# Optimization experiments

Hardware: AMD Instinct MI355X
Metric: run time of the kernel (lower is better)

Reference implementation:

```python
import jax, jax.numpy as jnp
import numpy as np

B, HW, C, D = 8, 65536, 64, 64  # batch, seq (H*W), channels, d_model
H = W = 256


def setup_inputs() -> dict:
    key = jax.random.key(0)
    ks = jax.random.split(key, 16)
    s = lambda k, shape, scale=0.05: jax.random.normal(k, shape, dtype=jnp.float32) * scale
    return {
        "x": jax.random.normal(ks[0], (B, HW, C), dtype=jnp.float32),
        "freq_map": jax.random.uniform(ks[1], (B, 1, H, W), dtype=jnp.float32),
        # proj_in: Linear(C, D)
        "W_in": s(ks[2], (C, D)), "b_in": s(ks[3], (D,)),
        # SimplifiedMambaKernel: in_proj Linear(D, 2D)
        "W_ip": s(ks[4], (D, 2 * D)), "b_ip": s(ks[5], (2 * D,)),
        # depthwise Conv1d(D, D, k=3, padding=1, groups=D): weight [D,1,3]
        "conv_w": s(ks[6], (D, 1, 3)), "conv_b": s(ks[7], (D,)),
        # mamba out_proj Linear(D, D)
        "W_op": s(ks[8], (D, D)), "b_op": s(ks[9], (D,)),
        # gate_net: Linear(1,16) -> ReLU -> Linear(16,C) -> Sigmoid
        "W_g1": s(ks[10], (1, 16)), "b_g1": s(ks[11], (16,)),
        "W_g2": s(ks[12], (16, C)), "b_g2": s(ks[13], (C,)),
        # proj_out: Linear(D, C)
        "W_out": s(ks[14], (D, C)), "b_out": s(ks[15], (C,)),
    }


def _mamba_kernel(feat, W_ip, b_ip, conv_w, conv_b, W_op, b_op):
    # feat: [B, L, D]
    x_and_res = feat @ W_ip + b_ip                      # [B, L, 2D]
    x_branch, res_branch = jnp.split(x_and_res, 2, axis=-1)
    xb = jnp.transpose(x_branch, (0, 2, 1))             # [B, D, L]
    xb = jax.lax.conv_general_dilated(
        xb, conv_w, window_strides=(1,), padding=[(1, 1)],
        feature_group_count=conv_w.shape[0],
        dimension_numbers=("NCH", "OIH", "NCH"))
    xb = xb + conv_b[None, :, None]
    x_branch = jnp.transpose(xb, (0, 2, 1))             # [B, L, D]
    out = jax.nn.silu(x_branch) * jax.nn.silu(res_branch)
    return out @ W_op + b_op


def reference(x, freq_map, W_in, b_in, W_ip, b_ip, conv_w, conv_b,
              W_op, b_op, W_g1, b_g1, W_g2, b_g2, W_out, b_out):
    feat = x @ W_in + b_in                              # [B, L, D]
    feat = _mamba_kernel(feat, W_ip, b_ip, conv_w, conv_b, W_op, b_op)
    feat_out = feat @ W_out + b_out                     # [B, L, C]
    # freq_map [B,1,H,W] -> flatten(2).permute(0,2,1) -> [B, L, 1]
    freq_flat = freq_map.reshape(freq_map.shape[0], 1, -1).transpose(0, 2, 1)
    gate = jax.nn.sigmoid(jax.nn.relu(freq_flat @ W_g1 + b_g1) @ W_g2 + b_g2)
    return feat_out * gate
```

## Files before the change

### kernel.cpp

```cpp
#include <hip/hip_runtime.h>
#include <hip/hip_bf16.h>

#define L_SEQ 65536
#define GROUPS_PER_B 256

typedef __attribute__((ext_vector_type(8))) short bf16x8;
typedef __attribute__((ext_vector_type(4))) short s16x4;
typedef __attribute__((ext_vector_type(4))) float f32x4;

#define WS_WFX   0
#define WS_W1R   24576
#define WS_W2T   32768
#define WS_WG2T  40960
#define WS_BX    43008
#define WS_BR    43264
#define WS_BC0   43520
#define WS_BC2   43776
#define WS_B2    44032

__device__ __forceinline__ short f2bf(float f) {
    __bf16 h = (__bf16)f;
    return __builtin_bit_cast(short, h);
}
__device__ __forceinline__ float fsigmoid(float x) {
    return __builtin_amdgcn_rcpf(1.0f + __builtin_amdgcn_exp2f(-1.44269504089f * x));
}

__global__ void prep_kernel(const float* __restrict__ W_in, const float* __restrict__ b_in,
                            const float* __restrict__ W_ip, const float* __restrict__ b_ip,
                            const float* __restrict__ conv_w, const float* __restrict__ conv_b,
                            const float* __restrict__ W_op, const float* __restrict__ b_op,
                            const float* __restrict__ W_g2,
                            const float* __restrict__ W_out, const float* __restrict__ b_out,
                            void* __restrict__ ws)
{
    short* wfx  = (short*)((char*)ws + WS_WFX);
    short* w1r  = (short*)((char*)ws + WS_W1R);
    short* w2t  = (short*)((char*)ws + WS_W2T);
    short* wg2t = (short*)((char*)ws + WS_WG2T);
    float* bx   = (float*)((char*)ws + WS_BX);
    float* br   = (float*)((char*)ws + WS_BR);
    float* bc0  = (float*)((char*)ws + WS_BC0);
    float* bc2  = (float*)((char*)ws + WS_BC2);
    float* b2   = (float*)((char*)ws + WS_B2);

    int tid = blockIdx.x * blockDim.x + threadIdx.x;
    if (tid < 12288) {
        int s = tid >> 12, rem = tid & 4095;
        int d = rem >> 6, c = rem & 63;
        float acc = 0.f;
        for (int e = 0; e < 64; ++e) acc += W_in[c*64 + e] * W_ip[e*128 + d];
        wfx[(s*64 + d)*64 + c] = f2bf(acc * conv_w[3*d + s]);
    } else if (tid < 16384) {
        int rem = tid - 12288; int d = rem >> 6, c = rem & 63;
        float acc = 0.f;
        for (int e = 0; e < 64; ++e) acc += W_in[c*64 + e] * W_ip[e*128 + 64 + d];
        w1r[d*64 + c] = f2bf(acc);
    } else if (tid < 20480) {
        int rem = tid - 16384; int cp = rem >> 6, d = rem & 63;
        float acc = 0.f;
        for (int e = 0; e < 64; ++e) acc += W_op[d*64 + e] * W_out[e*64 + cp];
        w2t[cp*64 + d] = f2bf(acc);
    } else if (tid < 21504) {
        int rem = tid - 20480; int c = rem >> 4, j = rem & 15;
        wg2t[c*16 + j] = f2bf(W_g2[j*64 + c]);
    } else if (tid < 21568) {
        int d = tid - 21504;
        float b1x = b_ip[d];
        for (int e = 0; e < 64; ++e) b1x += b_in[e] * W_ip[e*128 + d];
        bx[d] = b1x * (conv_w[3*d] + conv_w[3*d+1] + conv_w[3*d+2]) + conv_b[d];
    } else if (tid < 21632) {
        int d = tid - 21568;
        float s = b_ip[64 + d];
        for (int e = 0; e < 64; ++e) s += b_in[e] * W_ip[e*128 + 64 + d];
        br[d] = s;
    } else if (tid < 21696) {
        int d = tid - 21632;
        float b1x = b_ip[d];
        for (int e = 0; e < 64; ++e) b1x += b_in[e] * W_ip[e*128 + d];
        bc0[d] = b1x * conv_w[3*d];
    } else if (tid < 21760) {
        int d = tid - 21696;
        float b1x = b_ip[d];
        for (int e = 0; e < 64; ++e) b1x += b_in[e] * W_ip[e*128 + d];
        bc2[d] = b1x * conv_w[3*d + 2];
    } else if (tid < 21824) {
        int cp = tid - 21760;
        float s = b_out[cp];
        for (int e = 0; e < 64; ++e) s += b_op[e] * W_out[e*64 + cp];
        b2[cp] = s;
    }
}

__global__ __launch_bounds__(256, 4) void fgs_main(
    const float* __restrict__ x, const float* __restrict__ freq,
    const float* __restrict__ wg1, const float* __restrict__ bg1,
    const float* __restrict__ bg2,
    const void* __restrict__ ws, float* __restrict__ out)
{
    const short* wfx  = (const short*)((const char*)ws + WS_WFX);
    const short* w1r  = (const short*)((const char*)ws + WS_W1R);
    const short* w2t  = (const short*)((const char*)ws + WS_W2T);
    const short* wg2t = (const short*)((const char*)ws + WS_WG2T);
    const float* bxv  = (const float*)((const char*)ws + WS_BX);
    const float* brv  = (const float*)((const char*)ws + WS_BR);
    const float* bc0  = (const float*)((const char*)ws + WS_BC0);
    const float* bc2  = (const float*)((const char*)ws + WS_BC2);
    const float* b2   = (const float*)((const char*)ws + WS_B2);

    __shared__ short xs[2][66 * 64];
    __shared__ short ot[64][72];
    __shared__ short hl[2][64 * 16];

    const int bid   = blockIdx.x;
    const int batch = bid >> 8;
    const int tg    = bid & 255;
    const int base0 = tg << 8;

    const int lane = threadIdx.x & 63;
    const int w    = threadIdx.x >> 6;
    const int lr   = lane & 15;
    const int g    = lane >> 4;
    const int r    = 16*w + lr;
    const int c0   = 16*w + 4*g;

    const size_t brow0 = (size_t)batch * L_SEQ;

    bf16x8 awf[2][3], awr[2];
    #pragma unroll
    for (int kk = 0; kk < 2; ++kk) {
        #pragma unroll
        for (int s = 0; s < 3; ++s)
            awf[kk][s] = *(const bf16x8*)(wfx + (s*64 + 16*w + lr)*64 + 32*kk + 8*g);
        awr[kk] = *(const bf16x8*)(w1r + (16*w + lr)*64 + 32*kk + 8*g);
    }
    const float4 bbx = *(const float4*)(bxv + c0);
    const float4 bbr = *(const float4*)(brv + c0);
    const float4 wgv = *(const float4*)(wg1 + 4*g);
    const float4 bgv = *(const float4*)(bg1 + 4*g);

    float4 sa, sb, sc, sd; float sf;
    const int sro = threadIdx.x >> 2;
    const int sq  = (threadIdx.x & 3) * 16;

    auto stage_issue = [&](int tb) {
        int grow = tb + 1 + sro;
        bool v = ((unsigned)grow < (unsigned)L_SEQ);
        const float* p = x + (brow0 + (size_t)(v ? grow : 0)) * 64 + sq;
        sa = *(const float4*)(p);
        sb = *(const float4*)(p + 4);
        sc = *(const float4*)(p + 8);
        sd = *(const float4*)(p + 12);
        sf = freq[brow0 + tb + r];
    };
    auto stage_write = [&](short* xb, int tb) {
        int i = 2 + sro;
        int grow = tb + 1 + sro;
        bool v = ((unsigned)grow < (unsigned)L_SEQ);
        bf16x8 lo, hi;
        lo[0]=f2bf(sa.x); lo[1]=f2bf(sa.y); lo[2]=f2bf(sa.z); lo[3]=f2bf(sa.w);
        lo[4]=f2bf(sb.x); lo[5]=f2bf(sb.y); lo[6]=f2bf(sb.z); lo[7]=f2bf(sb.w);
        hi[0]=f2bf(sc.x); hi[1]=f2bf(sc.y); hi[2]=f2bf(sc.z); hi[3]=f2bf(sc.w);
        hi[4]=f2bf(sd.x); hi[5]=f2bf(sd.y); hi[6]=f2bf(sd.z); hi[7]=f2bf(sd.w);
        if (!v) { bf16x8 z = {}; lo = z; hi = z; }
        int cb = sq >> 3;
        int sw = i & 7;
        *(bf16x8*)&xb[i*64 + ((cb    ) ^ sw) * 8] = lo;
        *(bf16x8*)&xb[i*64 + ((cb + 1) ^ sw) * 8] = hi;
    };
    auto halo_copy = [&](short* xb, const short* xprev) {
        if (threadIdx.x < 16) {
            int ii = threadIdx.x >> 3;
            int cc = threadIdx.x & 7;
            *(bf16x8*)&xb[ii*64 + cc*8] = *(const bf16x8*)&xprev[(64 + ii)*64 + cc*8];
        }
    };
    auto hl_write = [&](short* hb) {
        s16x4 hv;
        hv[0] = f2bf(fmaxf(sf*wgv.x + bgv.x, 0.f));
        hv[1] = f2bf(fmaxf(sf*wgv.y + bgv.y, 0.f));
        hv[2] = f2bf(fmaxf(sf*wgv.z + bgv.z, 0.f));
        hv[3] = f2bf(fmaxf(sf*wgv.w + bgv.w, 0.f));
        *(s16x4*)&hb[r*16 + 4*g] = hv;
    };

    stage_issue(base0);
    if (threadIdx.x < 8) {
        int i = threadIdx.x >> 2;
        int grow = base0 - 1 + i;
        bool v = (grow >= 0);
        const float* p = x + (brow0 + (size_t)(v ? grow : 0)) * 64 + sq;
        float4 a = *(const float4*)(p);
        float4 b = *(const float4*)(p + 4);
        float4 c = *(const float4*)(p + 8);
        float4 d = *(const float4*)(p + 12);
        bf16x8 lo, hi;
        lo[0]=f2bf(a.x); lo[1]=f2bf(a.y); lo[2]=f2bf(a.z); lo[3]=f2bf(a.w);
        lo[4]=f2bf(b.x); lo[5]=f2bf(b.y); lo[6]=f2bf(b.z); lo[7]=f2bf(b.w);
        hi[0]=f2bf(c.x); hi[1]=f2bf(c.y); hi[2]=f2bf(c.z); hi[3]=f2bf(c.w);
        hi[4]=f2bf(d.x); hi[5]=f2bf(d.y); hi[6]=f2bf(d.z); hi[7]=f2bf(d.w);
        if (!v) { bf16x8 z = {}; lo = z; hi = z; }
        int cb = sq >> 3;
        int sw = i & 7;
        *(bf16x8*)&xs[0][i*64 + ((cb    ) ^ sw) * 8] = lo;
        *(bf16x8*)&xs[0][i*64 + ((cb + 1) ^ sw) * 8] = hi;
    }
    stage_write(xs[0], base0);
    hl_write(hl[0]);
    __syncthreads();

    #pragma unroll
    for (int t = 0; t < 4; ++t) {
        const int tb = base0 + (t << 6);
        short* xcur = xs[t & 1];
        short* xnxt = xs[(t & 1) ^ 1];
        short* hcur = hl[t & 1];
        short* hnxt = hl[(t & 1) ^ 1];

        if (t < 3) stage_issue(tb + 64);

        f32x4 accx[4] = {};
        f32x4 accr[4] = {};
        #pragma unroll
        for (int kk = 0; kk < 2; ++kk) {
            #pragma unroll
            for (int s = 0; s < 3; ++s) {
                int rb = lr + s;
                const short* bp = xcur + rb*64 + (((4*kk + g) ^ (rb & 7)) * 8);
                bf16x8 b0 = *(const bf16x8*)(bp);
                bf16x8 b1v = *(const bf16x8*)(bp + 1024);
                bf16x8 b2v = *(const bf16x8*)(bp + 2048);
                bf16x8 b3v = *(const bf16x8*)(bp + 3072);
                accx[0] = __builtin_amdgcn_mfma_f32_16x16x32_bf16(awf[kk][s], b0,  accx[0], 0, 0, 0);
                accx[1] = __builtin_amdgcn_mfma_f32_16x16x32_bf16(awf[kk][s], b1v, accx[1], 0, 0, 0);
                accx[2] = __builtin_amdgcn_mfma_f32_16x16x32_bf16(awf[kk][s], b2v, accx[2], 0, 0, 0);
                accx[3] = __builtin_amdgcn_mfma_f32_16x16x32_bf16(awf[kk][s], b3v, accx[3], 0, 0, 0);
                if (s == 1) {
                    accr[0] = __builtin_amdgcn_mfma_f32_16x16x32_bf16(awr[kk], b0,  accr[0], 0, 0, 0);
                    accr[1] = __builtin_amdgcn_mfma_f32_16x16x32_bf16(awr[kk], b1v, accr[1], 0, 0, 0);
                    accr[2] = __builtin_amdgcn_mfma_f32_16x16x32_bf16(awr[kk], b2v, accr[2], 0, 0, 0);
                    accr[3] = __builtin_amdgcn_mfma_f32_16x16x32_bf16(awr[kk], b3v, accr[3], 0, 0, 0);
                }
            }
        }

        #pragma unroll
        for (int nt = 0; nt < 4; ++nt) {
            int trow = 16*nt + lr;
            f32x4 vx = accx[nt];
            f32x4 vr = accr[nt];
            vx[0] += bbx.x; vx[1] += bbx.y; vx[2] += bbx.z; vx[3] += bbx.w;
            vr[0] += bbr.x; vr[1] += bbr.y; vr[2] += bbr.z; vr[3] += bbr.w;
            if (t == 0 && nt == 0 && tg == 0 && lr == 0) {
                float4 cc = *(const float4*)(bc0 + c0);
                vx[0] -= cc.x; vx[1] -= cc.y; vx[2] -= cc.z; vx[3] -= cc.w;
            }
            if (t == 3 && nt == 3 && tg == 255 && lr == 15) {
                float4 cc = *(const float4*)(bc2 + c0);
                vx[0] -= cc.x; vx[1] -= cc.y; vx[2] -= cc.z; vx[3] -= cc.w;
            }
            s16x4 pv;
            #pragma unroll
            for (int j = 0; j < 4; ++j) {
                float xx = vx[j], rr = vr[j];
                float ex = __builtin_amdgcn_exp2f(-1.44269504089f * xx);
                float er = __builtin_amdgcn_exp2f(-1.44269504089f * rr);
                float o = xx * rr * __builtin_amdgcn_rcpf((1.0f + ex) * (1.0f + er));
                pv[j] = f2bf(o);
            }
            *(s16x4*)&ot[trow][c0] = pv;
        }
        __syncthreads();

        if (t < 3) {
            stage_write(xnxt, tb + 64);
            halo_copy(xnxt, xcur);
            hl_write(hnxt);
        }

        bf16x8 a2_0 = *(const bf16x8*)(w2t + (16*w + lr)*64 + 8*g);
        bf16x8 a2_1 = *(const bf16x8*)(w2t + (16*w + lr)*64 + 32 + 8*g);
        bf16x8 zf = {};
        bf16x8 ag = (g < 2) ? *(const bf16x8*)(wg2t + (16*w + lr)*16 + 8*g) : zf;
        f32x4 acc2[4] = {};
        f32x4 accg[4] = {};
        #pragma unroll
        for (int nt = 0; nt < 4; ++nt) {
            int row = 16*nt + lr;
            bf16x8 bo0 = *(bf16x8*)&ot[row][8*g];
            bf16x8 bo1 = *(bf16x8*)&ot[row][32 + 8*g];
            bf16x8 bh  = (g < 2) ? *(bf16x8*)&hcur[row*16 + 8*g] : zf;
            acc2[nt] = __builtin_amdgcn_mfma_f32_16x16x32_bf16(a2_0, bo0, acc2[nt], 0, 0, 0);
            acc2[nt] = __builtin_amdgcn_mfma_f32_16x16x32_bf16(a2_1, bo1, acc2[nt], 0, 0, 0);
            accg[nt] = __builtin_amdgcn_mfma_f32_16x16x32_bf16(ag,   bh,  accg[nt], 0, 0, 0);
        }

        {
            float4 bb2 = *(const float4*)(b2 + c0);
            float4 bbg = *(const float4*)(bg2 + c0);
            float* op0 = out + (brow0 + (size_t)(tb + lr)) * 64 + c0;
            #pragma unroll
            for (int nt = 0; nt < 4; ++nt) {
                f32x4 y = acc2[nt], gg = accg[nt];
                float4 o;
                o.x = (y[0] + bb2.x) * fsigmoid(gg[0] + bbg.x);
                o.y = (y[1] + bb2.y) * fsigmoid(gg[1] + bbg.y);
                o.z = (y[2] + bb2.z) * fsigmoid(gg[2] + bbg.z);
                o.w = (y[3] + bb2.w) * fsigmoid(gg[3] + bbg.w);
                *(float4*)(op0 + (size_t)(nt << 4) * 64) = o;
            }
        }
        if (t < 3) __syncthreads();
    }
}

extern "C" void kernel_launch(void* const* d_in, const int* in_sizes, int n_in,
                              void* d_out, int out_size, void* d_ws, size_t ws_size,
                              hipStream_t stream)
{
    const float* x      = (const float*)d_in[0];
    const float* freq   = (const float*)d_in[1];
    const float* W_in   = (const float*)d_in[2];
    const float* b_in   = (const float*)d_in[3];
    const float* W_ip   = (const float*)d_in[4];
    const float* b_ip   = (const float*)d_in[5];
    const float* conv_w = (const float*)d_in[6];
    const float* conv_b = (const float*)d_in[7];
    const float* W_op   = (const float*)d_in[8];
    const float* b_op   = (const float*)d_in[9];
    const float* W_g1   = (const float*)d_in[10];
    const float* b_g1   = (const float*)d_in[11];
    const float* W_g2   = (const float*)d_in[12];
    const float* b_g2   = (const float*)d_in[13];
    const float* W_out  = (const float*)d_in[14];
    const float* b_out  = (const float*)d_in[15];
    float* out = (float*)d_out;

    prep_kernel<<<86, 256, 0, stream>>>(W_in, b_in, W_ip, b_ip, conv_w, conv_b,
                                        W_op, b_op, W_g2, W_out, b_out, d_ws);
    fgs_main<<<8 * GROUPS_PER_B, 256, 0, stream>>>(x, freq, W_g1, b_g1, b_g2, d_ws, out);
}
```

Measured before the change: 95.47 us.

## Halve per-block tile, single-buffer LDS, compute gate hidden in registers for occupancy

Each block now handles 128 rows instead of 256, and the grid grows to 4096 blocks. The LDS x tile is single-buffered and the hidden-gate LDS buffer is removed. The relu(freq*W_g1+b_g1) operand is now computed directly in registers. Weight fragments are reloaded from global or L1 inside the loop instead of being held in registers, launch bounds rise to 6 blocks per SIMD group, and the ot buffer switches from padding to XOR swizzling. The aim is lower LDS and register use so more blocks can be resident and hide memory latency, at the cost of halo reloads from global memory, repeated weight loads and less overlap between staging and compute.

```diff
diff --git a/kernel.cpp b/kernel.cpp
--- a/kernel.cpp
+++ b/kernel.cpp
@@ -2,7 +2,6 @@
 #include <hip/hip_bf16.h>
 
 #define L_SEQ 65536
-#define GROUPS_PER_B 256
 
 typedef __attribute__((ext_vector_type(8))) short bf16x8;
 typedef __attribute__((ext_vector_type(4))) short s16x4;
@@ -92,7 +91,7 @@
     }
 }
 
-__global__ __launch_bounds__(256, 4) void fgs_main(
+__global__ __launch_bounds__(256, 6) void fgs_main(
     const float* __restrict__ x, const float* __restrict__ freq,
     const float* __restrict__ wg1, const float* __restrict__ bg1,
     const float* __restrict__ bg2,
@@ -108,42 +107,29 @@
     const float* bc2  = (const float*)((const char*)ws + WS_BC2);
     const float* b2   = (const float*)((const char*)ws + WS_B2);
 
-    __shared__ short xs[2][66 * 64];
-    __shared__ short ot[64][72];
-    __shared__ short hl[2][64 * 16];
+    __shared__ short xs[66 * 64];
+    __shared__ short ot[64 * 64];
 
     const int bid   = blockIdx.x;
-    const int batch = bid >> 8;
-    const int tg    = bid & 255;
-    const int base0 = tg << 8;
+    const int batch = bid >> 9;
+    const int tg    = bid & 511;
+    const int base0 = tg << 7;
 
     const int lane = threadIdx.x & 63;
     const int w    = threadIdx.x >> 6;
     const int lr   = lane & 15;
     const int g    = lane >> 4;
-    const int r    = 16*w + lr;
     const int c0   = 16*w + 4*g;
 
     const size_t brow0 = (size_t)batch * L_SEQ;
 
-    bf16x8 awf[2][3], awr[2];
-    #pragma unroll
-    for (int kk = 0; kk < 2; ++kk) {
-        #pragma unroll
-        for (int s = 0; s < 3; ++s)
-            awf[kk][s] = *(const bf16x8*)(wfx + (s*64 + 16*w + lr)*64 + 32*kk + 8*g);
-        awr[kk] = *(const bf16x8*)(w1r + (16*w + lr)*64 + 32*kk + 8*g);
-    }
-    const float4 bbx = *(const float4*)(bxv + c0);
-    const float4 bbr = *(const float4*)(brv + c0);
-    const float4 wgv = *(const float4*)(wg1 + 4*g);
-    const float4 bgv = *(const float4*)(bg1 + 4*g);
-
-    float4 sa, sb, sc, sd; float sf;
     const int sro = threadIdx.x >> 2;
-    const int sq  = (threadIdx.x & 3) * 16;
-
-    auto stage_issue = [&](int tb) {
+    const int sq  = (threadIdx.x & 3) << 4;
+
+    float4 sa, sb, sc, sd;
+    f32x4 ff0 = {}, ff1 = {};
+
+    auto stage_issue = [&](int tb, f32x4* ffp) {
         int grow = tb + 1 + sro;
         bool v = ((unsigned)grow < (unsigned)L_SEQ);
         const float* p = x + (brow0 + (size_t)(v ? grow : 0)) * 64 + sq;
@@ -151,9 +137,13 @@
         sb = *(const float4*)(p + 4);
         sc = *(const float4*)(p + 8);
         sd = *(const float4*)(p + 12);
-        sf = freq[brow0 + tb + r];
+        f32x4 f;
+        #pragma unroll
+        for (int nt = 0; nt < 4; ++nt)
+            f[nt] = freq[brow0 + tb + 16*nt + lr];
+        *ffp = f;
     };
-    auto stage_write = [&](short* xb, int tb) {
+    auto stage_write = [&](int tb) {
         int i = 2 + sro;
         int grow = tb + 1 + sro;
         bool v = ((unsigned)grow < (unsigned)L_SEQ);
@@ -163,61 +153,45 @@
         hi[0]=f2bf(sc.x); hi[1]=f2bf(sc.y); hi[2]=f2bf(sc.z); hi[3]=f2bf(sc.w);
         hi[4]=f2bf(sd.x); hi[5]=f2bf(sd.y); hi[6]=f2bf(sd.z); hi[7]=f2bf(sd.w);
         if (!v) { bf16x8 z = {}; lo = z; hi = z; }
-        int cb = sq >> 3;
+        int cb = (threadIdx.x & 3) << 1;
         int sw = i & 7;
-        *(bf16x8*)&xb[i*64 + ((cb    ) ^ sw) * 8] = lo;
-        *(bf16x8*)&xb[i*64 + ((cb + 1) ^ sw) * 8] = hi;
+        *(bf16x8*)&xs[i*64 + ((cb       ^ sw) << 3)] = lo;
+        *(bf16x8*)&xs[i*64 + (((cb + 1) ^ sw) << 3)] = hi;
     };
-    auto halo_copy = [&](short* xb, const short* xprev) {
-        if (threadIdx.x < 16) {
-            int ii = threadIdx.x >> 3;
-            int cc = threadIdx.x & 7;
-            *(bf16x8*)&xb[ii*64 + cc*8] = *(const bf16x8*)&xprev[(64 + ii)*64 + cc*8];
+    auto halo_stage = [&](int tb) {
+        if (threadIdx.x < 8) {
+            int i = threadIdx.x >> 2;
+            int grow = tb - 1 + i;
+            bool v = (grow >= 0);
+            const float* p = x + (brow0 + (size_t)(v ? grow : 0)) * 64 + sq;
+            float4 a = *(const float4*)(p);
+            float4 b = *(const float4*)(p + 4);
+            float4 c = *(const float4*)(p + 8);
+            float4 d = *(const float4*)(p + 12);
+            bf16x8 lo, hi;
+            lo[0]=f2bf(a.x); lo[1]=f2bf(a.y); lo[2]=f2bf(a.z); lo[3]=f2bf(a.w);
+            lo[4]=f2bf(b.x); lo[5]=f2bf(b.y); lo[6]=f2bf(b.z); lo[7]=f2bf(b.w);
+            hi[0]=f2bf(c.x); hi[1]=f2bf(c.y); hi[2]=f2bf(c.z); hi[3]=f2bf(c.w);
+            hi[4]=f2bf(d.x); hi[5]=f2bf(d.y); hi[6]=f2bf(d.z); hi[7]=f2bf(d.w);
+            if (!v) { bf16x8 z = {}; lo = z; hi = z; }
+            int cb = (threadIdx.x & 3) << 1;
+            int sw = i & 7;
+            *(bf16x8*)&xs[i*64 + ((cb       ^ sw) << 3)] = lo;
+            *(bf16x8*)&xs[i*64 + (((cb + 1) ^ sw) << 3)] = hi;
         }
     };
-    auto hl_write = [&](short* hb) {
-        s16x4 hv;
-        hv[0] = f2bf(fmaxf(sf*wgv.x + bgv.x, 0.f));
-        hv[1] = f2bf(fmaxf(sf*wgv.y + bgv.y, 0.f));
-        hv[2] = f2bf(fmaxf(sf*wgv.z + bgv.z, 0.f));
-        hv[3] = f2bf(fmaxf(sf*wgv.w + bgv.w, 0.f));
-        *(s16x4*)&hb[r*16 + 4*g] = hv;
-    };
-
-    stage_issue(base0);
-    if (threadIdx.x < 8) {
-        int i = threadIdx.x >> 2;
-        int grow = base0 - 1 + i;
-        bool v = (grow >= 0);
-        const float* p = x + (brow0 + (size_t)(v ? grow : 0)) * 64 + sq;
-        float4 a = *(const float4*)(p);
-        float4 b = *(const float4*)(p + 4);
-        float4 c = *(const float4*)(p + 8);
-        float4 d = *(const float4*)(p + 12);
-        bf16x8 lo, hi;
-        lo[0]=f2bf(a.x); lo[1]=f2bf(a.y); lo[2]=f2bf(a.z); lo[3]=f2bf(a.w);
-        lo[4]=f2bf(b.x); lo[5]=f2bf(b.y); lo[6]=f2bf(b.z); lo[7]=f2bf(b.w);
-        hi[0]=f2bf(c.x); hi[1]=f2bf(c.y); hi[2]=f2bf(c.z); hi[3]=f2bf(c.w);
-        hi[4]=f2bf(d.x); hi[5]=f2bf(d.y); hi[6]=f2bf(d.z); hi[7]=f2bf(d.w);
-        if (!v) { bf16x8 z = {}; lo = z; hi = z; }
-        int cb = sq >> 3;
-        int sw = i & 7;
-        *(bf16x8*)&xs[0][i*64 + ((cb    ) ^ sw) * 8] = lo;
-        *(bf16x8*)&xs[0][i*64 + ((cb + 1) ^ sw) * 8] = hi;
-    }
-    stage_write(xs[0], base0);
-    hl_write(hl[0]);
+
+    stage_issue(base0, &ff0);
+    halo_stage(base0);
+    stage_write(base0);
     __syncthreads();
 
+    stage_issue(base0 + 64, &ff1);
+
     #pragma unroll
-    for (int t = 0; t < 4; ++t) {
+    for (int t = 0; t < 2; ++t) {
         const int tb = base0 + (t << 6);
-        short* xcur = xs[t & 1];
-        short* xnxt = xs[(t & 1) ^ 1];
-        short* hcur = hl[t & 1];
-        short* hnxt = hl[(t & 1) ^ 1];
-
-        if (t < 3) stage_issue(tb + 64);
+        const f32x4 ffv = t ? ff1 : ff0;
 
         f32x4 accx[4] = {};
         f32x4 accr[4] = {};
@@ -225,71 +199,96 @@
         for (int kk = 0; kk < 2; ++kk) {
             #pragma unroll
             for (int s = 0; s < 3; ++s) {
+                bf16x8 a = *(const bf16x8*)(wfx + (s*64 + 16*w + lr)*64 + 32*kk + 8*g);
                 int rb = lr + s;
-                const short* bp = xcur + rb*64 + (((4*kk + g) ^ (rb & 7)) * 8);
-                bf16x8 b0 = *(const bf16x8*)(bp);
+                const short* bp = xs + rb*64 + (((4*kk + g) ^ (rb & 7)) << 3);
+                bf16x8 b0  = *(const bf16x8*)(bp);
                 bf16x8 b1v = *(const bf16x8*)(bp + 1024);
                 bf16x8 b2v = *(const bf16x8*)(bp + 2048);
                 bf16x8 b3v = *(const bf16x8*)(bp + 3072);
-                accx[0] = __builtin_amdgcn_mfma_f32_16x16x32_bf16(awf[kk][s], b0,  accx[0], 0, 0, 0);
-                accx[1] = __builtin_amdgcn_mfma_f32_16x16x32_bf16(awf[kk][s], b1v, accx[1], 0, 0, 0);
-                accx[2] = __builtin_amdgcn_mfma_f32_16x16x32_bf16(awf[kk][s], b2v, accx[2], 0, 0, 0);
-                accx[3] = __builtin_amdgcn_mfma_f32_16x16x32_bf16(awf[kk][s], b3v, accx[3], 0, 0, 0);
+                accx[0] = __builtin_amdgcn_mfma_f32_16x16x32_bf16(a, b0,  accx[0], 0, 0, 0);
+                accx[1] = __builtin_amdgcn_mfma_f32_16x16x32_bf16(a, b1v, accx[1], 0, 0, 0);
+                accx[2] = __builtin_amdgcn_mfma_f32_16x16x32_bf16(a, b2v, accx[2], 0, 0, 0);
+                accx[3] = __builtin_amdgcn_mfma_f32_16x16x32_bf16(a, b3v, accx[3], 0, 0, 0);
                 if (s == 1) {
-                    accr[0] = __builtin_amdgcn_mfma_f32_16x16x32_bf16(awr[kk], b0,  accr[0], 0, 0, 0);
-                    accr[1] = __builtin_amdgcn_mfma_f32_16x16x32_bf16(awr[kk], b1v, accr[1], 0, 0, 0);
-                    accr[2] = __builtin_amdgcn_mfma_f32_16x16x32_bf16(awr[kk], b2v, accr[2], 0, 0, 0);
-                    accr[3] = __builtin_amdgcn_mfma_f32_16x16x32_bf16(awr[kk], b3v, accr[3], 0, 0, 0);
+                    bf16x8 ar = *(const bf16x8*)(w1r + (16*w + lr)*64 + 32*kk + 8*g);
+                    accr[0] = __builtin_amdgcn_mfma_f32_16x16x32_bf16(ar, b0,  accr[0], 0, 0, 0);
+                    accr[1] = __builtin_amdgcn_mfma_f32_16x16x32_bf16(ar, b1v, accr[1], 0, 0, 0);
+                    accr[2] = __builtin_amdgcn_mfma_f32_16x16x32_bf16(ar, b2v, accr[2], 0, 0, 0);
+                    accr[3] = __builtin_amdgcn_mfma_f32_16x16x32_bf16(ar, b3v, accr[3], 0, 0, 0);
                 }
             }
         }
 
-        #pragma unroll
-        for (int nt = 0; nt < 4; ++nt) {
-            int trow = 16*nt + lr;
-            f32x4 vx = accx[nt];
-            f32x4 vr = accr[nt];
-            vx[0] += bbx.x; vx[1] += bbx.y; vx[2] += bbx.z; vx[3] += bbx.w;
-            vr[0] += bbr.x; vr[1] += bbr.y; vr[2] += bbr.z; vr[3] += bbr.w;
-            if (t == 0 && nt == 0 && tg == 0 && lr == 0) {
-                float4 cc = *(const float4*)(bc0 + c0);
-                vx[0] -= cc.x; vx[1] -= cc.y; vx[2] -= cc.z; vx[3] -= cc.w;
+        {
+            const int ch  = c0 >> 3;
+            const int sub = c0 & 7;
+            float4 bbx = *(const float4*)(bxv + c0);
+            float4 bbr = *(const float4*)(brv + c0);
+            #pragma unroll
+            for (int nt = 0; nt < 4; ++nt) {
+                int trow = 16*nt + lr;
+                int grow = tb + trow;
+                f32x4 vx = accx[nt];
+                f32x4 vr = accr[nt];
+                vx[0] += bbx.x; vx[1] += bbx.y; vx[2] += bbx.z; vx[3] += bbx.w;
+                vr[0] += bbr.x; vr[1] += bbr.y; vr[2] += bbr.z; vr[3] += bbr.w;
+                if (grow == 0) {
+                    float4 cc = *(const float4*)(bc0 + c0);
+                    vx[0] -= cc.x; vx[1] -= cc.y; vx[2] -= cc.z; vx[3] -= cc.w;
+                }
+                if (grow == L_SEQ - 1) {
+                    float4 cc = *(const float4*)(bc2 + c0);
+                    vx[0] -= cc.x; vx[1] -= cc.y; vx[2] -= cc.z; vx[3] -= cc.w;
+                }
+                s16x4 pv;
+                #pragma unroll
+                for (int j = 0; j < 4; ++j) {
+                    float xx = vx[j], rr = vr[j];
+                    float ex = __builtin_amdgcn_exp2f(-1.44269504089f * xx);
+                    float er = __builtin_amdgcn_exp2f(-1.44269504089f * rr);
+                    float o = xx * rr * __builtin_amdgcn_rcpf((1.0f + ex) * (1.0f + er));
+                    pv[j] = f2bf(o);
+                }
+                *(s16x4*)&ot[trow*64 + ((ch ^ (trow & 7)) << 3) + sub] = pv;
             }
-            if (t == 3 && nt == 3 && tg == 255 && lr == 15) {
-                float4 cc = *(const float4*)(bc2 + c0);
-                vx[0] -= cc.x; vx[1] -= cc.y; vx[2] -= cc.z; vx[3] -= cc.w;
-            }
-            s16x4 pv;
-            #pragma unroll
-            for (int j = 0; j < 4; ++j) {
-                float xx = vx[j], rr = vr[j];
-                float ex = __builtin_amdgcn_exp2f(-1.44269504089f * xx);
-                float er = __builtin_amdgcn_exp2f(-1.44269504089f * rr);
-                float o = xx * rr * __builtin_amdgcn_rcpf((1.0f + ex) * (1.0f + er));
-                pv[j] = f2bf(o);
-            }
-            *(s16x4*)&ot[trow][c0] = pv;
         }
         __syncthreads();
 
-        if (t < 3) {
-            stage_write(xnxt, tb + 64);
-            halo_copy(xnxt, xcur);
-            hl_write(hnxt);
+        if (t == 0) {
+            stage_write(tb + 64);
+            halo_stage(tb + 64);
         }
 
         bf16x8 a2_0 = *(const bf16x8*)(w2t + (16*w + lr)*64 + 8*g);
         bf16x8 a2_1 = *(const bf16x8*)(w2t + (16*w + lr)*64 + 32 + 8*g);
         bf16x8 zf = {};
         bf16x8 ag = (g < 2) ? *(const bf16x8*)(wg2t + (16*w + lr)*16 + 8*g) : zf;
+        float4 wga = *(const float4*)(wg1 + 8*(g & 1));
+        float4 wgb = *(const float4*)(wg1 + 8*(g & 1) + 4);
+        float4 bga = *(const float4*)(bg1 + 8*(g & 1));
+        float4 bgb = *(const float4*)(bg1 + 8*(g & 1) + 4);
+
         f32x4 acc2[4] = {};
         f32x4 accg[4] = {};
         #pragma unroll
         for (int nt = 0; nt < 4; ++nt) {
             int row = 16*nt + lr;
-            bf16x8 bo0 = *(bf16x8*)&ot[row][8*g];
-            bf16x8 bo1 = *(bf16x8*)&ot[row][32 + 8*g];
-            bf16x8 bh  = (g < 2) ? *(bf16x8*)&hcur[row*16 + 8*g] : zf;
+            const short* orow = ot + row*64;
+            bf16x8 bo0 = *(const bf16x8*)(orow + ((g       ^ (row & 7)) << 3));
+            bf16x8 bo1 = *(const bf16x8*)(orow + (((4 + g) ^ (row & 7)) << 3));
+            bf16x8 bh = zf;
+            if (g < 2) {
+                float fv = ffv[nt];
+                bh[0] = f2bf(fmaxf(fv*wga.x + bga.x, 0.f));
+                bh[1] = f2bf(fmaxf(fv*wga.y + bga.y, 0.f));
+                bh[2] = f2bf(fmaxf(fv*wga.z + bga.z, 0.f));
+                bh[3] = f2bf(fmaxf(fv*wga.w + bga.w, 0.f));
+                bh[4] = f2bf(fmaxf(fv*wgb.x + bgb.x, 0.f));
+                bh[5] = f2bf(fmaxf(fv*wgb.y + bgb.y, 0.f));
+                bh[6] = f2bf(fmaxf(fv*wgb.z + bgb.z, 0.f));
+                bh[7] = f2bf(fmaxf(fv*wgb.w + bgb.w, 0.f));
+            }
             acc2[nt] = __builtin_amdgcn_mfma_f32_16x16x32_bf16(a2_0, bo0, acc2[nt], 0, 0, 0);
             acc2[nt] = __builtin_amdgcn_mfma_f32_16x16x32_bf16(a2_1, bo1, acc2[nt], 0, 0, 0);
             accg[nt] = __builtin_amdgcn_mfma_f32_16x16x32_bf16(ag,   bh,  accg[nt], 0, 0, 0);
@@ -310,7 +309,8 @@
                 *(float4*)(op0 + (size_t)(nt << 4) * 64) = o;
             }
         }
-        if (t < 3) __syncthreads();
+
+        if (t == 0) __syncthreads();
     }
 }
 
@@ -338,5 +338,5 @@
 
     prep_kernel<<<86, 256, 0, stream>>>(W_in, b_in, W_ip, b_ip, conv_w, conv_b,
                                         W_op, b_op, W_g2, W_out, b_out, d_ws);
-    fgs_main<<<8 * GROUPS_PER_B, 256, 0, stream>>>(x, freq, W_g1, b_g1, b_g2, d_ws, out);
-}
+    fgs_main<<<8 * 512, 256, 0, stream>>>(x, freq, W_g1, b_g1, b_g2, d_ws, out);
+}
```

Result: slower. 140.4 us (+47.0%).
